# Kernel tuning notes

Measured on AMD Instinct MI355X. Metric: run time of the kernel, lower is better.

The kernel has to match this reference:

```python
import jax, jax.numpy as jnp
import numpy as np

N = 20000   # nodes
D = 512     # input_dim
H = 256     # hidden_dim = input_dim // 2
C = 7       # class_num
L = 2       # layer_num
E = 131072  # edges per class
B = 8192    # edge pairs to classify
EPS = 1e-5  # BatchNorm eps


def _bn(x, gamma, beta):
    # BatchNorm1d in training mode: batch mean / biased variance
    mu = jnp.mean(x, axis=0)
    var = jnp.mean((x - mu) ** 2, axis=0)
    return (x - mu) * jax.lax.rsqrt(var + EPS) * gamma + beta


def _gcn_conv(x, src, dst, W, b):
    # PyG GCNConv: add self-loops, symmetric deg^-1/2 normalization, aggregate at dst
    n = x.shape[0]
    loop = jnp.arange(n)
    s = jnp.concatenate([src, loop])
    d = jnp.concatenate([dst, loop])
    deg = jax.ops.segment_sum(jnp.ones(s.shape[0], x.dtype), d, num_segments=n)
    dinv = jax.lax.rsqrt(jnp.maximum(deg, 1.0))  # deg >= 1 due to self-loops
    norm = dinv[s] * dinv[d]                     # [E+N]
    xw = x @ W                                   # [N, H]
    out = jax.ops.segment_sum(norm[:, None] * xw[s], d, num_segments=n)
    return out + b


def _comp_gcn(x, edge_index, gW, gb, dW, db):
    row, col = edge_index[0], edge_index[1]
    h = jax.nn.relu(_gcn_conv(x, row, col, gW, gb))
    comp = (x[col] * x[row]) @ dW + db           # diff_proj(x[col]*x[row])
    msg = jax.ops.segment_sum(comp, row, num_segments=x.shape[0])
    return h + msg


def setup_inputs() -> dict:
    key = jax.random.key(0)
    ks = jax.random.split(key, 20)
    s = 0.05
    nrm = lambda k, shape: jax.random.normal(k, shape, jnp.float32) * s
    return {
        "x": jax.random.normal(ks[0], (N, D), jnp.float32),
        "edges": jax.random.randint(ks[1], (C, 2, E), 0, N),
        "node_id": jax.random.randint(ks[2], (2, B), 0, N),
        "lin0_W": nrm(ks[3], (C, D, H)),
        "lin0_b": nrm(ks[4], (C, H)),
        "bn_gamma": jnp.ones((C, H), jnp.float32),
        "bn_beta": jnp.zeros((C, H), jnp.float32),
        "gcn_W": nrm(ks[5], (C, L, H, H)),
        "gcn_b": nrm(ks[6], (C, L, H)),
        "dp_W": nrm(ks[7], (C, L, H, H)),
        "dp_b": nrm(ks[8], (C, L, H)),
        "fc1_W": nrm(ks[9], (C, 3 * H, 3 * H // 2)),
        "fc1_b": nrm(ks[10], (C, 3 * H // 2)),
        "fc2_W": nrm(ks[11], (C, 3 * H // 2, 3 * H // 4)),
        "fc2_b": nrm(ks[12], (C, 3 * H // 4)),
        "fc3_W": nrm(ks[13], (C, 3 * H // 4, H // 16)),
        "fc3_b": nrm(ks[14], (C, H // 16)),
        "cls_W": nrm(ks[15], ((H // 16) * C, C)),
        "cls_b": nrm(ks[16], (C,)),
    }


def reference(x, edges, node_id, lin0_W, lin0_b, bn_gamma, bn_beta,
              gcn_W, gcn_b, dp_W, dp_b, fc1_W, fc1_b, fc2_W, fc2_b,
              fc3_W, fc3_b, cls_W, cls_b):
    src, dst = node_id[0], node_id[1]
    outs = []
    for i in range(C):  # fixed small branch count
        t = jax.nn.relu(_bn(x @ lin0_W[i] + lin0_b[i], bn_gamma[i], bn_beta[i]))
        for j in range(L):
            t = _comp_gcn(t, edges[i], gcn_W[i, j], gcn_b[i, j], dp_W[i, j], dp_b[i, j])
        x1, x2 = t[src], t[dst]                        # [B, H]
        p = jnp.concatenate([x1, x2, x1 * x2], axis=1)  # [B, 3H]
        p = jax.nn.relu(p @ fc1_W[i] + fc1_b[i])
        p = jax.nn.relu(p @ fc2_W[i] + fc2_b[i])
        p = p @ fc3_W[i] + fc3_b[i]                     # [B, H//16]
        outs.append(p)
    r = jax.nn.relu(jnp.concatenate(outs, axis=1))      # [B, C*H//16]
    return r @ cls_W + cls_b                            # [B, C]
```

## Files before the change

### kernel.cpp

```cpp
#include <hip/hip_runtime.h>

typedef unsigned short u16;
typedef unsigned int   u32;
typedef __attribute__((ext_vector_type(8))) short short8;
typedef __attribute__((ext_vector_type(4))) float f32x4;

#define NNODES 20000
#define MPAD   20096
#define DIN    512
#define HID    256
#define NCLS   7
#define NLAY   2
#define NEDGE  131072
#define NPAIR  8192
#define BN_EPS 1e-5f

__device__ __forceinline__ void atomAddF(float* p, float v) { unsafeAtomicAdd(p, v); }

__device__ __forceinline__ float b2f(u16 u) {
    u32 x = ((u32)u) << 16;
    return __builtin_bit_cast(float, x);
}
__device__ __forceinline__ u16 f2b(float f) {
    u32 u = __builtin_bit_cast(u32, f);
    u32 r = u + 0x7FFFu + ((u >> 16) & 1u);
    return (u16)(r >> 16);
}
__device__ __forceinline__ float4 b2f4(ushort4 u) {
    return make_float4(b2f(u.x), b2f(u.y), b2f(u.z), b2f(u.w));
}
__device__ __forceinline__ ushort4 f2b4(float a, float b, float c, float d) {
    ushort4 o; o.x = f2b(a); o.y = f2b(b); o.z = f2b(c); o.w = f2b(d); return o;
}

__device__ __forceinline__ void async_copy16(const u16* g, u16* l) {
    __builtin_amdgcn_global_load_lds((const __attribute__((address_space(1))) void*)g,
                                     (__attribute__((address_space(3))) void*)l, 16, 0, 0);
}

__device__ __forceinline__ int chunk_swz(int orig, int nwg) {
    int xcd = orig & 7, q = nwg >> 3, r = nwg & 7;
    int base = (xcd < r) ? xcd * (q + 1) : r * (q + 1) + (xcd - r) * q;
    return base + (orig >> 3);
}

__global__ __launch_bounds__(256, 2) void gemm_fn(
    const u16* __restrict__ A, size_t sA, const u16* __restrict__ Bt, size_t sB,
    const float* __restrict__ bias, int sBias,
    float* __restrict__ Cf, u16* __restrict__ Cb, size_t sC,
    int M, int N, int K, int relu)
{
    const int z = blockIdx.z;
    A  += (size_t)z * sA;
    Bt += (size_t)z * sB;
    if (bias) bias += (size_t)z * sBias;

    __shared__ u16 sm[12288];
    u16* As = sm;
    u16* Bs = sm + 4096;

    const int tid  = threadIdx.x;
    const int wave = tid >> 6;
    const int lane = tid & 63;
    const int bm = blockIdx.x * 128;
    const int wr = (wave >> 1) * 64;
    const int wc = (wave & 1) * 128;

    const int ar = tid >> 2, aj = (tid & 3) * 8;
    const u16* AgA = A + (size_t)(bm + ar) * K + aj;
    const u16* AgB = A + (size_t)(bm + ar + 64) * K + aj;
    u16* AsA = As + tid * 8;
    u16* AsB = As + tid * 8 + 2048;
    const u16* BgC[4]; u16* BsC[4];
    #pragma unroll
    for (int c = 0; c < 4; ++c) {
        BgC[c] = Bt + (size_t)(c * 64 + ar) * K + aj;
        BsC[c] = Bs + ((size_t)c * 256 + tid) * 8;
    }

    const int fr = lane & 15;
    const int fq = lane >> 4;
    const int kg = fq * 8;

    f32x4 zero = {0.f, 0.f, 0.f, 0.f};
    f32x4 acc[4][8];
    #pragma unroll
    for (int mi = 0; mi < 4; ++mi)
        #pragma unroll
        for (int ni = 0; ni < 8; ++ni) acc[mi][ni] = zero;

    for (int k0 = 0; k0 < K; k0 += 32) {
        async_copy16(AgA + k0, AsA);
        async_copy16(AgB + k0, AsB);
        #pragma unroll
        for (int c = 0; c < 4; ++c) async_copy16(BgC[c] + k0, BsC[c]);
        __syncthreads();
        short8 af[4], bfr[8];
        #pragma unroll
        for (int mi = 0; mi < 4; ++mi)
            af[mi] = *(const short8*)&As[(wr + mi * 16 + fr) * 32 + kg];
        #pragma unroll
        for (int ni = 0; ni < 8; ++ni)
            bfr[ni] = *(const short8*)&Bs[(wc + ni * 16 + fr) * 32 + kg];
        #pragma unroll
        for (int mi = 0; mi < 4; ++mi)
            #pragma unroll
            for (int ni = 0; ni < 8; ++ni)
                acc[mi][ni] = __builtin_amdgcn_mfma_f32_16x16x32_bf16(
                    af[mi], bfr[ni], acc[mi][ni], 0, 0, 0);
        __syncthreads();
    }

    float bv[8];
    #pragma unroll
    for (int ni = 0; ni < 8; ++ni) {
        int col = wc + ni * 16 + fr;
        bv[ni] = (bias && col < N) ? bias[col] : 0.f;
    }

    if (Cb && N == 256) {
        u16* R = sm;
        const int lrb = (wave >> 1) * 16 + fq * 4;
        const int cb0 = wc + fr;
        #pragma unroll
        for (int mi = 0; mi < 4; ++mi) {
            __syncthreads();
            #pragma unroll
            for (int ni = 0; ni < 8; ++ni)
                #pragma unroll
                for (int rr = 0; rr < 4; ++rr) {
                    float v = acc[mi][ni][rr] + bv[ni];
                    if (relu) v = fmaxf(v, 0.f);
                    R[(lrb + rr) * 264 + cb0 + ni * 16] = f2b(v);
                }
            __syncthreads();
            #pragma unroll
            for (int p = 0; p < 4; ++p) {
                int idx = p * 256 + tid;
                int lr = idx >> 5, ch = idx & 31;
                int grow = bm + (lr >> 4) * 64 + mi * 16 + (lr & 15);
                if (grow < M)
                    *(short8*)&Cb[(size_t)z * sC + (size_t)grow * 256 + ch * 8] =
                        *(const short8*)&R[lr * 264 + ch * 8];
            }
        }
    } else {
        #pragma unroll
        for (int ni = 0; ni < 8; ++ni) {
            int col = wc + ni * 16 + fr;
            if (col >= N) continue;
            #pragma unroll
            for (int mi = 0; mi < 4; ++mi) {
                int rbase = bm + wr + mi * 16 + fq * 4;
                #pragma unroll
                for (int rr = 0; rr < 4; ++rr) {
                    int row = rbase + rr;
                    if (row >= M) continue;
                    float v = acc[mi][ni][rr] + bv[ni];
                    if (relu) v = fmaxf(v, 0.f);
                    size_t o = (size_t)z * sC + (size_t)row * N + col;
                    if (Cf) Cf[o] = v;
                    if (Cb) Cb[o] = f2b(v);
                }
            }
        }
    }
}

__global__ __launch_bounds__(256, 2) void gemm_dual(
    const u16* U, const u16* __restrict__ V, size_t sAct,
    const u16* __restrict__ Gt, const u16* __restrict__ Dt, size_t sW,
    const float* __restrict__ gbias, const float* __restrict__ dbias, int sBias,
    const float* __restrict__ degf, size_t sDeg,
    u16* Cb, int M)
{
    const int z = blockIdx.z;
    U += (size_t)z * sAct; V += (size_t)z * sAct;
    Gt += (size_t)z * sW;  Dt += (size_t)z * sW;
    gbias += (size_t)z * sBias; dbias += (size_t)z * sBias;
    degf  += (size_t)z * sDeg;
    u16* C = Cb + (size_t)z * sAct;

    __shared__ u16 sm[12288];
    u16* As = sm;
    u16* Bs = sm + 4096;

    const int tid  = threadIdx.x;
    const int wave = tid >> 6;
    const int lane = tid & 63;
    const int bm = blockIdx.x * 128;
    const int wr = (wave >> 1) * 64;
    const int wc = (wave & 1) * 128;

    const int ar = tid >> 2, aj = (tid & 3) * 8;
    u16* AsA = As + tid * 8;
    u16* AsB = As + tid * 8 + 2048;

    const int fr = lane & 15;
    const int fq = lane >> 4;
    const int kg = fq * 8;

    f32x4 zero = {0.f, 0.f, 0.f, 0.f};
    f32x4 acc[4][8];
    #pragma unroll
    for (int mi = 0; mi < 4; ++mi)
        #pragma unroll
        for (int ni = 0; ni < 8; ++ni) acc[mi][ni] = zero;

    for (int k0 = 0; k0 < HID; k0 += 32) {
        async_copy16(U + (size_t)(bm + ar) * HID + aj + k0, AsA);
        async_copy16(U + (size_t)(bm + ar + 64) * HID + aj + k0, AsB);
        #pragma unroll
        for (int c = 0; c < 4; ++c)
            async_copy16(Gt + (size_t)(c * 64 + ar) * HID + aj + k0,
                         Bs + ((size_t)c * 256 + tid) * 8);
        __syncthreads();
        short8 af[4], bfr[8];
        #pragma unroll
        for (int mi = 0; mi < 4; ++mi)
            af[mi] = *(const short8*)&As[(wr + mi * 16 + fr) * 32 + kg];
        #pragma unroll
        for (int ni = 0; ni < 8; ++ni)
            bfr[ni] = *(const short8*)&Bs[(wc + ni * 16 + fr) * 32 + kg];
        #pragma unroll
        for (int mi = 0; mi < 4; ++mi)
            #pragma unroll
            for (int ni = 0; ni < 8; ++ni)
                acc[mi][ni] = __builtin_amdgcn_mfma_f32_16x16x32_bf16(
                    af[mi], bfr[ni], acc[mi][ni], 0, 0, 0);
        __syncthreads();
    }

    {
        float gv[8];
        #pragma unroll
        for (int ni = 0; ni < 8; ++ni) gv[ni] = gbias[wc + ni * 16 + fr];
        #pragma unroll
        for (int mi = 0; mi < 4; ++mi)
            #pragma unroll
            for (int ni = 0; ni < 8; ++ni)
                #pragma unroll
                for (int rr = 0; rr < 4; ++rr)
                    acc[mi][ni][rr] = fmaxf(acc[mi][ni][rr] + gv[ni], 0.f);
    }

    for (int k0 = 0; k0 < HID; k0 += 32) {
        async_copy16(V + (size_t)(bm + ar) * HID + aj + k0, AsA);
        async_copy16(V + (size_t)(bm + ar + 64) * HID + aj + k0, AsB);
        #pragma unroll
        for (int c = 0; c < 4; ++c)
            async_copy16(Dt + (size_t)(c * 64 + ar) * HID + aj + k0,
                         Bs + ((size_t)c * 256 + tid) * 8);
        __syncthreads();
        short8 af[4], bfr[8];
        #pragma unroll
        for (int mi = 0; mi < 4; ++mi)
            af[mi] = *(const short8*)&As[(wr + mi * 16 + fr) * 32 + kg];
        #pragma unroll
        for (int ni = 0; ni < 8; ++ni)
            bfr[ni] = *(const short8*)&Bs[(wc + ni * 16 + fr) * 32 + kg];
        #pragma unroll
        for (int mi = 0; mi < 4; ++mi)
            #pragma unroll
            for (int ni = 0; ni < 8; ++ni)
                acc[mi][ni] = __builtin_amdgcn_mfma_f32_16x16x32_bf16(
                    af[mi], bfr[ni], acc[mi][ni], 0, 0, 0);
        __syncthreads();
    }

    float dv8[8];
    #pragma unroll
    for (int ni = 0; ni < 8; ++ni) dv8[ni] = dbias[wc + ni * 16 + fr];
    u16* R = sm;
    const int lrb = (wave >> 1) * 16 + fq * 4;
    const int cb0 = wc + fr;
    #pragma unroll
    for (int mi = 0; mi < 4; ++mi) {
        __syncthreads();
        float dgr[4];
        #pragma unroll
        for (int rr = 0; rr < 4; ++rr) {
            int grow = bm + wr + mi * 16 + fq * 4 + rr;
            dgr[rr] = (grow < M) ? degf[grow] : 0.f;
        }
        #pragma unroll
        for (int ni = 0; ni < 8; ++ni)
            #pragma unroll
            for (int rr = 0; rr < 4; ++rr)
                R[(lrb + rr) * 264 + cb0 + ni * 16] =
                    f2b(acc[mi][ni][rr] + dgr[rr] * dv8[ni]);
        __syncthreads();
        #pragma unroll
        for (int p = 0; p < 4; ++p) {
            int idx = p * 256 + tid;
            int lr = idx >> 5, ch = idx & 31;
            int grow = bm + (lr >> 4) * 64 + mi * 16 + (lr & 15);
            if (grow < M)
                *(short8*)&C[(size_t)grow * 256 + ch * 8] =
                    *(const short8*)&R[lr * 264 + ch * 8];
        }
    }
}

__global__ __launch_bounds__(256) void fc1_fused(
    const u16* __restrict__ tb, const int* __restrict__ src, const int* __restrict__ dst,
    const u16* __restrict__ Wt, const float* __restrict__ bias, u16* __restrict__ p1b)
{
    const int z = blockIdx.z;
    const u16* T = tb + (size_t)z * NNODES * HID;
    const u16* Bt = Wt + (size_t)z * 384 * 768;
    const float* bi = bias + (size_t)z * 384;
    u16* C = p1b + (size_t)z * NPAIR * 384;

    __shared__ u16 As[128 * 32];
    __shared__ u16 Bs[128 * 32];
    const int tid  = threadIdx.x;
    const int wave = tid >> 6;
    const int lane = tid & 63;
    const int bm = blockIdx.x * 128;
    const int bn = blockIdx.y * 128;
    const int wr = (wave >> 1) * 64;
    const int wc = (wave & 1) * 64;

    const int srow = wave * 32 + (lane >> 2);
    const int scol = (lane & 3) * 8;
    const int b0 = bm + srow, b1 = b0 + 16;
    const int s0i = src[b0], d0i = dst[b0];
    const int s1i = src[b1], d1i = dst[b1];

    const u16* Bg0 = Bt + (size_t)(bn + srow) * 768 + scol;
    const u16* Bg1 = Bg0 + (size_t)16 * 768;
    u16* As0 = &As[wave * 1024];
    u16* As1 = As0 + 512;
    u16* Bs0 = &Bs[wave * 1024];
    u16* Bs1 = Bs0 + 512;
    u16* Aw0 = As0 + lane * 8;
    u16* Aw1 = As1 + lane * 8;

    const int fr = lane & 15;
    const int kg = (lane >> 4) * 8;

    f32x4 zero = {0.f, 0.f, 0.f, 0.f};
    f32x4 acc[4][4];
    #pragma unroll
    for (int mi = 0; mi < 4; ++mi)
        #pragma unroll
        for (int ni = 0; ni < 4; ++ni) acc[mi][ni] = zero;

    for (int k0 = 0; k0 < 768; k0 += 32) {
        if (k0 < 512) {
            const u16* r0p = (k0 < 256) ? (T + (size_t)s0i * HID + k0 + scol)
                                        : (T + (size_t)d0i * HID + (k0 - 256) + scol);
            const u16* r1p = (k0 < 256) ? (T + (size_t)s1i * HID + k0 + scol)
                                        : (T + (size_t)d1i * HID + (k0 - 256) + scol);
            async_copy16(r0p, As0);
            async_copy16(r1p, As1);
        } else {
            int kk = k0 - 512 + scol;
            short8 a0 = *(const short8*)&T[(size_t)s0i * HID + kk];
            short8 c0 = *(const short8*)&T[(size_t)d0i * HID + kk];
            short8 a1 = *(const short8*)&T[(size_t)s1i * HID + kk];
            short8 c1 = *(const short8*)&T[(size_t)d1i * HID + kk];
            short8 p0, p1;
            #pragma unroll
            for (int j = 0; j < 8; ++j) {
                p0[j] = (short)f2b(b2f((u16)a0[j]) * b2f((u16)c0[j]));
                p1[j] = (short)f2b(b2f((u16)a1[j]) * b2f((u16)c1[j]));
            }
            *(short8*)Aw0 = p0;
            *(short8*)Aw1 = p1;
        }
        async_copy16(Bg0 + k0, Bs0);
        async_copy16(Bg1 + k0, Bs1);
        __syncthreads();
        short8 af[4], bfr[4];
        #pragma unroll
        for (int mi = 0; mi < 4; ++mi)
            af[mi] = *(const short8*)&As[(wr + mi * 16 + fr) * 32 + kg];
        #pragma unroll
        for (int ni = 0; ni < 4; ++ni)
            bfr[ni] = *(const short8*)&Bs[(wc + ni * 16 + fr) * 32 + kg];
        #pragma unroll
        for (int mi = 0; mi < 4; ++mi)
            #pragma unroll
            for (int ni = 0; ni < 4; ++ni)
                acc[mi][ni] = __builtin_amdgcn_mfma_f32_16x16x32_bf16(
                    af[mi], bfr[ni], acc[mi][ni], 0, 0, 0);
        __syncthreads();
    }

    const int fq = lane >> 4;
    #pragma unroll
    for (int ni = 0; ni < 4; ++ni) {
        int col = bn + wc + ni * 16 + fr;
        if (col >= 384) continue;
        float bz = bi[col];
        #pragma unroll
        for (int mi = 0; mi < 4; ++mi) {
            int rbase = bm + wr + mi * 16 + fq * 4;
            #pragma unroll
            for (int r = 0; r < 4; ++r) {
                int row = rbase + r;
                float v = fmaxf(acc[mi][ni][r] + bz, 0.f);
                C[(size_t)row * 384 + col] = f2b(v);
            }
        }
    }
}

#define TBM 64
#define TBN 64
#define TBK 16
__global__ void gemm_bias_b(const float* __restrict__ A, size_t sA,
                            const float* __restrict__ B, size_t sB,
                            const float* __restrict__ bias, int sBias,
                            float* __restrict__ C, size_t sC,
                            int M, int N, int K, int ldc, int relu)
{
    const int z = blockIdx.z;
    A += (size_t)z * sA; B += (size_t)z * sB;
    bias += (size_t)z * sBias; C += (size_t)z * sC;

    __shared__ float As[TBK][TBM + 1];
    __shared__ float Bs[TBK][TBN + 1];
    const int bm = blockIdx.x * TBM;
    const int bn = blockIdx.y * TBN;
    const int tid = threadIdx.x;
    const int tm = (tid / 16) * 4;
    const int tn = (tid % 16) * 4;
    float acc[4][4] = {};

    for (int k0 = 0; k0 < K; k0 += TBK) {
        #pragma unroll
        for (int l = 0; l < 4; ++l) {
            int idx = tid + l * 256;
            int m = idx / TBK, k = idx % TBK;
            int gm = bm + m;
            float v = 0.f;
            if (gm < M) v = A[(size_t)gm * K + k0 + k];
            As[k][m] = v;
        }
        #pragma unroll
        for (int l = 0; l < 4; ++l) {
            int idx = tid + l * 256;
            int k = idx / TBN, n = idx % TBN;
            int gn = bn + n;
            float v = 0.f;
            if (gn < N) v = B[(size_t)(k0 + k) * N + gn];
            Bs[k][n] = v;
        }
        __syncthreads();
        #pragma unroll
        for (int k = 0; k < TBK; ++k) {
            float a[4], b[4];
            #pragma unroll
            for (int i = 0; i < 4; ++i) a[i] = As[k][tm + i];
            #pragma unroll
            for (int j = 0; j < 4; ++j) b[j] = Bs[k][tn + j];
            #pragma unroll
            for (int i = 0; i < 4; ++i)
                #pragma unroll
                for (int j = 0; j < 4; ++j)
                    acc[i][j] = fmaf(a[i], b[j], acc[i][j]);
        }
        __syncthreads();
    }
    #pragma unroll
    for (int i = 0; i < 4; ++i) {
        int gm = bm + tm + i;
        if (gm >= M) continue;
        #pragma unroll
        for (int j = 0; j < 4; ++j) {
            int gn = bn + tn + j;
            if (gn >= N) continue;
            float v = acc[i][j] + bias[gn];
            if (relu) v = fmaxf(v, 0.f);
            C[(size_t)gm * ldc + gn] = v;
        }
    }
}

__global__ void xconv(const float* __restrict__ x, u16* __restrict__ xb)
{
    int gid = blockIdx.x * blockDim.x + threadIdx.x;
    int i4 = gid * 4;
    int row = i4 >> 9;
    float4 v = make_float4(0.f, 0.f, 0.f, 0.f);
    if (row < NNODES) v = *(const float4*)&x[i4];
    *(ushort4*)&xb[i4] = f2b4(v.x, v.y, v.z, v.w);
}

__global__ void wtrans(const float* __restrict__ W, u16* __restrict__ Wt,
                       int K, int N, int NP)
{
    __shared__ float tile[32][33];
    const int m = blockIdx.z;
    const int k0 = blockIdx.x * 32, n0 = blockIdx.y * 32;
    const float* Wm = W + (size_t)m * K * N;
    u16* Wtm = Wt + (size_t)m * NP * K;
    const int c = threadIdx.x & 31, r = threadIdx.x >> 5;
    #pragma unroll
    for (int p = 0; p < 4; ++p)
        tile[r + p * 8][c] = Wm[(size_t)(k0 + r + p * 8) * N + n0 + c];
    __syncthreads();
    #pragma unroll
    for (int p = 0; p < 4; ++p)
        Wtm[(size_t)(n0 + r + p * 8) * K + k0 + c] = f2b(tile[c][r + p * 8]);
}

__device__ __forceinline__ int swz3584(int b) { return (b & 7) * 448 + (b >> 3); }

__global__ void hist(const int* __restrict__ edges, int* __restrict__ ptrs)
{
    int gid = swz3584(blockIdx.x) * 256 + threadIdx.x;
    int i = gid >> 17, e = gid & (NEDGE - 1);
    const int* eb = edges + (size_t)i * 2 * NEDGE;
    int r = eb[e], c = eb[NEDGE + e];
    atomicAdd(&ptrs[i * 20001 + c + 1], 1);
    atomicAdd(&ptrs[(7 + i) * 20001 + r + 1], 1);
}

#define SCN 512
__global__ void scan1(int* __restrict__ ptrs, int* __restrict__ aux)
{
    __shared__ int s[SCN];
    const int a = blockIdx.y;
    const int t = threadIdx.x;
    const int idx = blockIdx.x * SCN + t;
    int* arr = ptrs + a * 20001;
    int v = (idx < 20001) ? arr[idx] : 0;
    s[t] = v;
    __syncthreads();
    for (int off = 1; off < SCN; off <<= 1) {
        int x = (t >= off) ? s[t - off] : 0;
        __syncthreads();
        s[t] += x;
        __syncthreads();
    }
    if (idx < 20001) arr[idx] = s[t];
    if (t == SCN - 1) aux[a * 40 + blockIdx.x] = s[t];
}
__global__ void scan2(int* __restrict__ aux)
{
    if (threadIdx.x != 0) return;
    int a = blockIdx.x;
    int run = 0;
    for (int b = 0; b < 40; ++b) {
        int t = aux[a * 40 + b];
        aux[a * 40 + b] = run;
        run += t;
    }
}
__global__ void scan3(int* __restrict__ ptrs, const int* __restrict__ aux,
                      int* __restrict__ cur)
{
    const int a = blockIdx.y;
    const int idx = blockIdx.x * SCN + threadIdx.x;
    if (idx < 20001) {
        int v = ptrs[a * 20001 + idx] + aux[a * 40 + blockIdx.x];
        ptrs[a * 20001 + idx] = v;
        cur[a * 20001 + idx] = v;
    }
}
__global__ void csrfill(const int* __restrict__ edges, int* __restrict__ cur,
                        int* __restrict__ othercol, int* __restrict__ otherrow)
{
    int gid = swz3584(blockIdx.x) * 256 + threadIdx.x;
    int i = gid >> 17, e = gid & (NEDGE - 1);
    const int* eb = edges + (size_t)i * 2 * NEDGE;
    int r = eb[e], c = eb[NEDGE + e];
    int pc = atomicAdd(&cur[i * 20001 + c], 1);
    othercol[(size_t)i * NEDGE + pc] = r;
    int pr = atomicAdd(&cur[(7 + i) * 20001 + r], 1);
    otherrow[(size_t)i * NEDGE + pr] = c;
}
__global__ void mkdinv(const int* __restrict__ ptrs, float* __restrict__ dinv,
                       float* __restrict__ degf)
{
    int gid = blockIdx.x * blockDim.x + threadIdx.x;
    if (gid >= NCLS * NNODES) return;
    int i = gid / NNODES, n = gid - i * NNODES;
    int d = ptrs[i * 20001 + n + 1] - ptrs[i * 20001 + n];
    dinv[gid] = rsqrtf((float)d + 1.0f);
    int dr = ptrs[(7 + i) * 20001 + n + 1] - ptrs[(7 + i) * 20001 + n];
    degf[gid] = (float)dr;
}

#define STAT_ROWS 128
__global__ void colstats_b(const u16* __restrict__ xwb, float* __restrict__ stats)
{
    const int z = blockIdx.y;
    const int f = threadIdx.x;
    const int r0 = blockIdx.x * STAT_ROWS;
    const int r1 = min(r0 + STAT_ROWS, NNODES);
    const u16* X = xwb + (size_t)z * NNODES * HID;
    float s = 0.f, sq = 0.f;
    for (int r = r0; r < r1; ++r) {
        float v = b2f(X[(size_t)r * HID + f]);
        s += v; sq += v * v;
    }
    atomAddF(&stats[z * 2 * HID + f], s);
    atomAddF(&stats[z * 2 * HID + HID + f], sq);
}
__global__ void bn_relu_b(const u16* __restrict__ xwb, const float* __restrict__ stats,
                          const float* __restrict__ gamma, const float* __restrict__ beta,
                          u16* __restrict__ tb)
{
    const int z = blockIdx.y;
    const int gid = blockIdx.x * blockDim.x + threadIdx.x;
    const int n = gid >> 6, f4 = (gid & 63) * 4;
    const u16* X = xwb + (size_t)z * NNODES * HID;
    u16* T = tb + (size_t)z * NNODES * HID;
    const float* st = stats + z * 2 * HID;
    const float invN = 1.0f / NNODES;
    float4 su = *(const float4*)&st[f4];
    float4 sq = *(const float4*)&st[HID + f4];
    float4 g  = *(const float4*)&gamma[(size_t)z * HID + f4];
    float4 be = *(const float4*)&beta[(size_t)z * HID + f4];
    ushort4 u = *(const ushort4*)&X[(size_t)n * HID + f4];
    float4 x = b2f4(u);
    float o[4], mu, var;
    mu = su.x * invN; var = sq.x * invN - mu * mu;
    o[0] = fmaxf((x.x - mu) * rsqrtf(var + BN_EPS) * g.x + be.x, 0.f);
    mu = su.y * invN; var = sq.y * invN - mu * mu;
    o[1] = fmaxf((x.y - mu) * rsqrtf(var + BN_EPS) * g.y + be.y, 0.f);
    mu = su.z * invN; var = sq.z * invN - mu * mu;
    o[2] = fmaxf((x.z - mu) * rsqrtf(var + BN_EPS) * g.z + be.z, 0.f);
    mu = su.w * invN; var = sq.w * invN - mu * mu;
    o[3] = fmaxf((x.w - mu) * rsqrtf(var + BN_EPS) * g.w + be.w, 0.f);
    *(ushort4*)&T[(size_t)n * HID + f4] = f2b4(o[0], o[1], o[2], o[3]);
}

__global__ void gather2_u4(const u16* __restrict__ tb,
                           const int* __restrict__ cptrs, const int* __restrict__ coth,
                           const int* __restrict__ rptrs, const int* __restrict__ roth,
                           const float* __restrict__ dinv,
                           u16* __restrict__ ub, u16* __restrict__ vb, int nwg)
{
    const int logical = chunk_swz(blockIdx.x, nwg);
    const int z = logical / 5000, nb = logical % 5000;
    const size_t zo = (size_t)z * NNODES;
    const u16* T = tb + zo * HID;
    const int* cptr = cptrs + (size_t)z * 20001;
    const int* rptr = rptrs + (size_t)z * 20001;
    const int* co = coth + (size_t)z * NEDGE;
    const int* ro = roth + (size_t)z * NEDGE;
    const float* dv = dinv + zo;

    const int node = nb * 4 + (threadIdx.x >> 6);
    const int f = (threadIdx.x & 63) * 4;
    const float dn = dv[node];
    ushort4 tn = *(const ushort4*)&T[(size_t)node * HID + f];
    const float tnx = b2f(tn.x), tny = b2f(tn.y), tnz = b2f(tn.z), tnw = b2f(tn.w);

    float ax = dn * tnx, ay = dn * tny, az = dn * tnz, aw = dn * tnw;
    {
        const int s0 = cptr[node], s1 = cptr[node + 1];
        int e = s0;
        for (; e + 4 <= s1; e += 4) {
            int r0 = co[e], r1 = co[e + 1], r2 = co[e + 2], r3 = co[e + 3];
            float d0 = dv[r0], d1 = dv[r1], d2 = dv[r2], d3 = dv[r3];
            ushort4 u0 = *(const ushort4*)&T[(size_t)r0 * HID + f];
            ushort4 u1 = *(const ushort4*)&T[(size_t)r1 * HID + f];
            ushort4 u2 = *(const ushort4*)&T[(size_t)r2 * HID + f];
            ushort4 u3 = *(const ushort4*)&T[(size_t)r3 * HID + f];
            ax += d0 * b2f(u0.x) + d1 * b2f(u1.x) + d2 * b2f(u2.x) + d3 * b2f(u3.x);
            ay += d0 * b2f(u0.y) + d1 * b2f(u1.y) + d2 * b2f(u2.y) + d3 * b2f(u3.y);
            az += d0 * b2f(u0.z) + d1 * b2f(u1.z) + d2 * b2f(u2.z) + d3 * b2f(u3.z);
            aw += d0 * b2f(u0.w) + d1 * b2f(u1.w) + d2 * b2f(u2.w) + d3 * b2f(u3.w);
        }
        for (; e < s1; ++e) {
            int r = co[e];
            float dr = dv[r];
            ushort4 u = *(const ushort4*)&T[(size_t)r * HID + f];
            ax += dr * b2f(u.x); ay += dr * b2f(u.y);
            az += dr * b2f(u.z); aw += dr * b2f(u.w);
        }
    }
    *(ushort4*)&ub[(zo + node) * HID + f] = f2b4(dn * ax, dn * ay, dn * az, dn * aw);

    float bx = 0.f, by = 0.f, bz = 0.f, bw = 0.f;
    {
        const int s0 = rptr[node], s1 = rptr[node + 1];
        int e = s0;
        for (; e + 4 <= s1; e += 4) {
            int r0 = ro[e], r1 = ro[e + 1], r2 = ro[e + 2], r3 = ro[e + 3];
            ushort4 u0 = *(const ushort4*)&T[(size_t)r0 * HID + f];
            ushort4 u1 = *(const ushort4*)&T[(size_t)r1 * HID + f];
            ushort4 u2 = *(const ushort4*)&T[(size_t)r2 * HID + f];
            ushort4 u3 = *(const ushort4*)&T[(size_t)r3 * HID + f];
            bx += b2f(u0.x) + b2f(u1.x) + b2f(u2.x) + b2f(u3.x);
            by += b2f(u0.y) + b2f(u1.y) + b2f(u2.y) + b2f(u3.y);
            bz += b2f(u0.z) + b2f(u1.z) + b2f(u2.z) + b2f(u3.z);
            bw += b2f(u0.w) + b2f(u1.w) + b2f(u2.w) + b2f(u3.w);
        }
        for (; e < s1; ++e) {
            int cc = ro[e];
            ushort4 u = *(const ushort4*)&T[(size_t)cc * HID + f];
            bx += b2f(u.x); by += b2f(u.y);
            bz += b2f(u.z); bw += b2f(u.w);
        }
    }
    *(ushort4*)&vb[(zo + node) * HID + f] = f2b4(tnx * bx, tny * by, tnz * bz, tnw * bw);
}

__global__ void final_cls(const float* __restrict__ outs, const float* __restrict__ clsW,
                          const float* __restrict__ clsb, float* __restrict__ out)
{
    const int gid = blockIdx.x * blockDim.x + threadIdx.x;
    if (gid >= NPAIR * NCLS) return;
    const int b = gid / NCLS, c = gid % NCLS;
    float acc = clsb[c];
    const float* row = outs + (size_t)b * 112;
    #pragma unroll 4
    for (int k = 0; k < 112; ++k)
        acc = fmaf(fmaxf(row[k], 0.f), clsW[k * NCLS + c], acc);
    out[gid] = acc;
}

extern "C" void kernel_launch(void* const* d_in, const int* in_sizes, int n_in,
                              void* d_out, int out_size, void* d_ws, size_t ws_size,
                              hipStream_t stream)
{
    const float* x        = (const float*)d_in[0];
    const int*   edges    = (const int*)  d_in[1];
    const int*   node_id  = (const int*)  d_in[2];
    const float* lin0_W   = (const float*)d_in[3];
    const float* lin0_b   = (const float*)d_in[4];
    const float* bn_gamma = (const float*)d_in[5];
    const float* bn_beta  = (const float*)d_in[6];
    const float* gcn_W    = (const float*)d_in[7];
    const float* gcn_b    = (const float*)d_in[8];
    const float* dp_W     = (const float*)d_in[9];
    const float* dp_b     = (const float*)d_in[10];
    const float* fc1_W    = (const float*)d_in[11];
    const float* fc1_b    = (const float*)d_in[12];
    const float* fc2_W    = (const float*)d_in[13];
    const float* fc2_b    = (const float*)d_in[14];
    const float* fc3_W    = (const float*)d_in[15];
    const float* fc3_b    = (const float*)d_in[16];
    const float* cls_W    = (const float*)d_in[17];
    const float* cls_b    = (const float*)d_in[18];
    float* out = (float*)d_out;

    unsigned char* w = (unsigned char*)d_ws;
    size_t used = 0;
    auto alloc = [&](size_t bytes) {
        void* p = (void*)(w + used);
        used += (bytes + 255) & ~(size_t)255;
        return p;
    };
    u16*   xb       = (u16*)  alloc((size_t)MPAD * DIN * 2);
    u16*   lin0Wt   = (u16*)  alloc((size_t)NCLS * HID * DIN * 2);
    u16*   gcnWt    = (u16*)  alloc((size_t)NCLS * NLAY * HID * HID * 2);
    u16*   dpWt     = (u16*)  alloc((size_t)NCLS * NLAY * HID * HID * 2);
    u16*   fc1Wt    = (u16*)  alloc((size_t)NCLS * 384 * 768 * 2);
    u16*   fc2Wt    = (u16*)  alloc((size_t)NCLS * 256 * 384 * 2);
    int*   ptrs     = (int*)  alloc((size_t)14 * 20001 * 4);
    int*   cur      = (int*)  alloc((size_t)14 * 20001 * 4);
    int*   aux      = (int*)  alloc((size_t)14 * 40 * 4);
    int*   othercol = (int*)  alloc((size_t)NCLS * NEDGE * 4);
    int*   otherrow = (int*)  alloc((size_t)NCLS * NEDGE * 4);
    float* dinv     = (float*)alloc((size_t)NCLS * NNODES * 4);
    float* degf     = (float*)alloc((size_t)NCLS * NNODES * 4);
    float* outsb    = (float*)alloc((size_t)NPAIR * 112 * 4);
    float* stats    = (float*)alloc((size_t)NCLS * 2 * HID * 4);

    int g = 1;
    for (int t = NCLS; t >= 1; --t) {
        size_t big = ((size_t)t * NNODES + 96) * HID * 2;
        big = (big + 255) & ~(size_t)255;
        if (used + 3 * big <= ws_size) { g = t; break; }
    }
    size_t bigBytes = ((size_t)g * NNODES + 96) * HID * 2;
    u16* tbA  = (u16*)alloc(bigBytes);
    u16* ubuf = (u16*)alloc(bigBytes);
    u16* vbuf = (u16*)alloc(bigBytes);
    u16*   p1b = ubuf;
    float* p2f = (float*)vbuf;

    const int* src = node_id;
    const int* dst = node_id + NPAIR;

    xconv<<<(MPAD * DIN / 4) / 256, 256, 0, stream>>>(x, xb);
    wtrans<<<dim3(16, 8, 7),  256, 0, stream>>>(lin0_W, lin0Wt, 512, 256, 256);
    wtrans<<<dim3(8, 8, 14),  256, 0, stream>>>(gcn_W,  gcnWt,  256, 256, 256);
    wtrans<<<dim3(8, 8, 14),  256, 0, stream>>>(dp_W,   dpWt,   256, 256, 256);
    wtrans<<<dim3(24, 12, 7), 256, 0, stream>>>(fc1_W,  fc1Wt,  768, 384, 384);
    wtrans<<<dim3(12, 6, 7),  256, 0, stream>>>(fc2_W,  fc2Wt,  384, 192, 256);

    hipMemsetAsync(ptrs, 0, (size_t)14 * 20001 * 4, stream);
    hist<<<(NCLS * NEDGE) / 256, 256, 0, stream>>>(edges, ptrs);
    scan1<<<dim3(40, 14), SCN, 0, stream>>>(ptrs, aux);
    scan2<<<14, 64, 0, stream>>>(aux);
    scan3<<<dim3(40, 14), SCN, 0, stream>>>(ptrs, aux, cur);
    csrfill<<<(NCLS * NEDGE) / 256, 256, 0, stream>>>(edges, cur, othercol, otherrow);
    mkdinv<<<(NCLS * NNODES + 255) / 256, 256, 0, stream>>>(ptrs, dinv, degf);

    const size_t sT = (size_t)NNODES * HID;

    for (int cb = 0; cb < NCLS; cb += g) {
        const int gl = min(g, NCLS - cb);
        const int nwg = gl * 5000;

        gemm_fn<<<dim3(157, 1, gl), 256, 0, stream>>>(
            xb, 0, lin0Wt + (size_t)cb * HID * DIN, (size_t)HID * DIN,
            lin0_b + cb * HID, HID, nullptr, ubuf, sT, NNODES, HID, DIN, 0);
        hipMemsetAsync(stats, 0, (size_t)gl * 2 * HID * 4, stream);
        colstats_b<<<dim3(157, gl), HID, 0, stream>>>(ubuf, stats);
        bn_relu_b<<<dim3(5000, gl), 256, 0, stream>>>(
            ubuf, stats, bn_gamma + cb * HID, bn_beta + cb * HID, tbA);

        u16* t_cur = tbA;
        u16* t_alt = ubuf;
        for (int j = 0; j < NLAY; ++j) {
            const u16* gWt = gcnWt + ((size_t)cb * NLAY + j) * HID * HID;
            const u16* dWt = dpWt  + ((size_t)cb * NLAY + j) * HID * HID;
            const float* gb = gcn_b + ((size_t)cb * NLAY + j) * HID;
            const float* db = dp_b  + ((size_t)cb * NLAY + j) * HID;

            gather2_u4<<<nwg, 256, 0, stream>>>(
                t_cur, ptrs + cb * 20001, othercol + (size_t)cb * NEDGE,
                ptrs + (7 + cb) * 20001, otherrow + (size_t)cb * NEDGE,
                dinv + (size_t)cb * NNODES, t_alt, vbuf, nwg);
            gemm_dual<<<dim3(157, 1, gl), 256, 0, stream>>>(
                t_alt, vbuf, sT, gWt, dWt, (size_t)NLAY * HID * HID,
                gb, db, NLAY * HID, degf + (size_t)cb * NNODES, (size_t)NNODES,
                t_alt, NNODES);

            u16* tmp = t_cur; t_cur = t_alt; t_alt = tmp;
        }

        fc1_fused<<<dim3(64, 3, gl), 256, 0, stream>>>(
            t_cur, src, dst, fc1Wt + (size_t)cb * 384 * 768, fc1_b + cb * 384, p1b);
        gemm_fn<<<dim3(64, 1, gl), 256, 0, stream>>>(
            p1b, (size_t)NPAIR * 384, fc2Wt + (size_t)cb * 256 * 384, (size_t)256 * 384,
            fc2_b + cb * 192, 192, p2f, nullptr, (size_t)NPAIR * 192,
            NPAIR, 192, 384, 1);
        gemm_bias_b<<<dim3(128, 1, gl), 256, 0, stream>>>(
            p2f, (size_t)NPAIR * 192, fc3_W + (size_t)cb * 192 * 16, (size_t)192 * 16,
            fc3_b + cb * 16, 16, outsb + cb * 16, 16,
            NPAIR, 16, 192, 112, 0);
    }

    final_cls<<<(NPAIR * NCLS + 255) / 256, 256, 0, stream>>>(outsb, cls_W, cls_b, out);
}
```

Before: 886.3 us.

## Fuse BatchNorm column stats into lin0 GEMM epilogue and shrink CSR indices to u16

Removes the separate colstats kernel by having the lin0 GEMM reduce per-column sum and sum of squares from its fp32 accumulators into shared memory, then atomically add them to global stats. It also stores the CSR neighbour indices as 16-bit values, since node ids stay below 65536, which halves index traffic in the gather kernel. The trade is extra shared atomics and syncs in the GEMM epilogue. Stats now come from fp32 values before bf16 rounding, so results shift slightly.

```diff
diff --git a/kernel.cpp b/kernel.cpp
--- a/kernel.cpp
+++ b/kernel.cpp
@@ -48,7 +48,7 @@
     const u16* __restrict__ A, size_t sA, const u16* __restrict__ Bt, size_t sB,
     const float* __restrict__ bias, int sBias,
     float* __restrict__ Cf, u16* __restrict__ Cb, size_t sC,
-    int M, int N, int K, int relu)
+    int M, int N, int K, int relu, float* statsOut)
 {
     const int z = blockIdx.z;
     A  += (size_t)z * sA;
@@ -56,6 +56,7 @@
     if (bias) bias += (size_t)z * sBias;
 
     __shared__ u16 sm[12288];
+    __shared__ float sred[512];
     u16* As = sm;
     u16* Bs = sm + 4096;
 
@@ -116,6 +117,31 @@
     for (int ni = 0; ni < 8; ++ni) {
         int col = wc + ni * 16 + fr;
         bv[ni] = (bias && col < N) ? bias[col] : 0.f;
+    }
+
+    if (statsOut) {
+        sred[tid] = 0.f; sred[256 + tid] = 0.f;
+        __syncthreads();
+        #pragma unroll
+        for (int ni = 0; ni < 8; ++ni) {
+            int col = wc + ni * 16 + fr;
+            float s = 0.f, sq = 0.f;
+            #pragma unroll
+            for (int mi = 0; mi < 4; ++mi)
+                #pragma unroll
+                for (int rr = 0; rr < 4; ++rr) {
+                    int row = bm + wr + mi * 16 + fq * 4 + rr;
+                    if (row < M) {
+                        float v = acc[mi][ni][rr] + bv[ni];
+                        s += v; sq += v * v;
+                    }
+                }
+            atomicAdd(&sred[col], s);
+            atomicAdd(&sred[256 + col], sq);
+        }
+        __syncthreads();
+        atomAddF(&statsOut[(size_t)z * 512 + tid], sred[tid]);
+        atomAddF(&statsOut[(size_t)z * 512 + 256 + tid], sred[256 + tid]);
     }
 
     if (Cb && N == 256) {
@@ -563,16 +589,16 @@
     }
 }
 __global__ void csrfill(const int* __restrict__ edges, int* __restrict__ cur,
-                        int* __restrict__ othercol, int* __restrict__ otherrow)
+                        u16* __restrict__ othercol, u16* __restrict__ otherrow)
 {
     int gid = swz3584(blockIdx.x) * 256 + threadIdx.x;
     int i = gid >> 17, e = gid & (NEDGE - 1);
     const int* eb = edges + (size_t)i * 2 * NEDGE;
     int r = eb[e], c = eb[NEDGE + e];
     int pc = atomicAdd(&cur[i * 20001 + c], 1);
-    othercol[(size_t)i * NEDGE + pc] = r;
+    othercol[(size_t)i * NEDGE + pc] = (u16)r;
     int pr = atomicAdd(&cur[(7 + i) * 20001 + r], 1);
-    otherrow[(size_t)i * NEDGE + pr] = c;
+    otherrow[(size_t)i * NEDGE + pr] = (u16)c;
 }
 __global__ void mkdinv(const int* __restrict__ ptrs, float* __restrict__ dinv,
                        float* __restrict__ degf)
@@ -586,22 +612,6 @@
     degf[gid] = (float)dr;
 }
 
-#define STAT_ROWS 128
-__global__ void colstats_b(const u16* __restrict__ xwb, float* __restrict__ stats)
-{
-    const int z = blockIdx.y;
-    const int f = threadIdx.x;
-    const int r0 = blockIdx.x * STAT_ROWS;
-    const int r1 = min(r0 + STAT_ROWS, NNODES);
-    const u16* X = xwb + (size_t)z * NNODES * HID;
-    float s = 0.f, sq = 0.f;
-    for (int r = r0; r < r1; ++r) {
-        float v = b2f(X[(size_t)r * HID + f]);
-        s += v; sq += v * v;
-    }
-    atomAddF(&stats[z * 2 * HID + f], s);
-    atomAddF(&stats[z * 2 * HID + HID + f], sq);
-}
 __global__ void bn_relu_b(const u16* __restrict__ xwb, const float* __restrict__ stats,
                           const float* __restrict__ gamma, const float* __restrict__ beta,
                           u16* __restrict__ tb)
@@ -632,8 +642,8 @@
 }
 
 __global__ void gather2_u4(const u16* __restrict__ tb,
-                           const int* __restrict__ cptrs, const int* __restrict__ coth,
-                           const int* __restrict__ rptrs, const int* __restrict__ roth,
+                           const int* __restrict__ cptrs, const u16* __restrict__ coth,
+                           const int* __restrict__ rptrs, const u16* __restrict__ roth,
                            const float* __restrict__ dinv,
                            u16* __restrict__ ub, u16* __restrict__ vb, int nwg)
 {
@@ -643,8 +653,8 @@
     const u16* T = tb + zo * HID;
     const int* cptr = cptrs + (size_t)z * 20001;
     const int* rptr = rptrs + (size_t)z * 20001;
-    const int* co = coth + (size_t)z * NEDGE;
-    const int* ro = roth + (size_t)z * NEDGE;
+    const u16* co = coth + (size_t)z * NEDGE;
+    const u16* ro = roth + (size_t)z * NEDGE;
     const float* dv = dinv + zo;
 
     const int node = nb * 4 + (threadIdx.x >> 6);
@@ -759,8 +769,8 @@
     int*   ptrs     = (int*)  alloc((size_t)14 * 20001 * 4);
     int*   cur      = (int*)  alloc((size_t)14 * 20001 * 4);
     int*   aux      = (int*)  alloc((size_t)14 * 40 * 4);
-    int*   othercol = (int*)  alloc((size_t)NCLS * NEDGE * 4);
-    int*   otherrow = (int*)  alloc((size_t)NCLS * NEDGE * 4);
+    u16*   othercol = (u16*)  alloc((size_t)NCLS * NEDGE * 2);
+    u16*   otherrow = (u16*)  alloc((size_t)NCLS * NEDGE * 2);
     float* dinv     = (float*)alloc((size_t)NCLS * NNODES * 4);
     float* degf     = (float*)alloc((size_t)NCLS * NNODES * 4);
     float* outsb    = (float*)alloc((size_t)NPAIR * 112 * 4);
@@ -803,11 +813,10 @@
         const int gl = min(g, NCLS - cb);
         const int nwg = gl * 5000;
 
+        hipMemsetAsync(stats, 0, (size_t)gl * 2 * HID * 4, stream);
         gemm_fn<<<dim3(157, 1, gl), 256, 0, stream>>>(
             xb, 0, lin0Wt + (size_t)cb * HID * DIN, (size_t)HID * DIN,
-            lin0_b + cb * HID, HID, nullptr, ubuf, sT, NNODES, HID, DIN, 0);
-        hipMemsetAsync(stats, 0, (size_t)gl * 2 * HID * 4, stream);
-        colstats_b<<<dim3(157, gl), HID, 0, stream>>>(ubuf, stats);
+            lin0_b + cb * HID, HID, nullptr, ubuf, sT, NNODES, HID, DIN, 0, stats);
         bn_relu_b<<<dim3(5000, gl), 256, 0, stream>>>(
             ubuf, stats, bn_gamma + cb * HID, bn_beta + cb * HID, tbA);
 
@@ -836,7 +845,7 @@
         gemm_fn<<<dim3(64, 1, gl), 256, 0, stream>>>(
             p1b, (size_t)NPAIR * 384, fc2Wt + (size_t)cb * 256 * 384, (size_t)256 * 384,
             fc2_b + cb * 192, 192, p2f, nullptr, (size_t)NPAIR * 192,
-            NPAIR, 192, 384, 1);
+            NPAIR, 192, 384, 1, nullptr);
         gemm_bias_b<<<dim3(128, 1, gl), 256, 0, stream>>>(
             p2f, (size_t)NPAIR * 192, fc3_W + (size_t)cb * 192 * 16, (size_t)192 * 16,
             fc3_b + cb * 16, 16, outsb + cb * 16, 16,
```

Measured after the change: 869.0 us, median of 2. 1.02x faster.
